# Kernel optimization log

Hardware: AMD Instinct MI355X
Metric: run time of the kernel (lower is better)

## Reference

```python
import jax, jax.numpy as jnp
import numpy as np
import math

B, S, D = 4, 2048, 1024

def setup_inputs() -> dict:
    key = jax.random.key(0)
    k1, k2, k3, k4 = jax.random.split(key, 4)
    scale = 1.0 / math.sqrt(D)
    return {
        "x": jax.random.normal(k1, (B, S, D), dtype=jnp.float32),
        "w_q": jax.random.normal(k2, (D, D), dtype=jnp.float32) * scale,
        "w_k": jax.random.normal(k3, (D, D), dtype=jnp.float32) * scale,
        "w_v": jax.random.normal(k4, (D, D), dtype=jnp.float32) * scale,
        "causal": 1,
    }

def reference(x, w_q, w_k, w_v, causal):
    # QKV projections: nn.Linear(dim, dim, bias=False) -> x @ W.T
    q = jnp.einsum('bsd,ed->bse', x, w_q)
    k = jnp.einsum('bsd,ed->bse', x, w_k)
    v = jnp.einsum('bsd,ed->bse', x, w_v)
    d_k = q.shape[-1]
    scores = jnp.einsum('bqd,bkd->bqk', q, k) / jnp.sqrt(jnp.asarray(d_k, q.dtype))
    if causal:
        seq_len = q.shape[-2]
        mask = jnp.triu(jnp.ones((seq_len, seq_len), dtype=bool), k=1)
        scores = jnp.where(mask, jnp.asarray(-jnp.inf, scores.dtype), scores)
    weights = jax.nn.softmax(scores, axis=-1)
    return jnp.einsum('bqk,bkd->bqd', weights, v)
```

## Files before the change

kernel.cpp:

```cpp
#include <hip/hip_runtime.h>
#include <stdint.h>

typedef unsigned short u16;
typedef __attribute__((ext_vector_type(8))) __bf16 bf16x8;
typedef __attribute__((ext_vector_type(4))) float f32x4;

__device__ __forceinline__ u16 f2bf(float f) {
  unsigned u = __float_as_uint(f);
  u += 0x7FFF + ((u >> 16) & 1);
  return (u16)(u >> 16);
}

__device__ __forceinline__ float bf2f(u16 h) {
  return __uint_as_float(((unsigned)h) << 16);
}

__device__ __forceinline__ void llds16(const u16* g, u16* l) {
  __builtin_amdgcn_global_load_lds(
      (const __attribute__((address_space(1))) void*)g,
      (__attribute__((address_space(3))) void*)l, 16, 0, 0);
}

__global__ __launch_bounds__(256) void cast_all(
    const float* __restrict__ x, const float* __restrict__ wq,
    const float* __restrict__ wk, const float* __restrict__ wv,
    u16* __restrict__ xb, u16* __restrict__ wb, float* __restrict__ lsum) {
  int i = blockIdx.x * 256 + threadIdx.x;
  if (i < 8192) lsum[i] = 0.f;
  const float* src; u16* dst; int off;
  if (i < 2097152)      { src = x;  dst = xb;            off = i; }
  else if (i < 2359296) { src = wq; dst = wb;            off = i - 2097152; }
  else if (i < 2621440) { src = wk; dst = wb + 1048576;  off = i - 2359296; }
  else                  { src = wv; dst = wb + 2097152;  off = i - 2621440; }
  float4 f = ((const float4*)src)[off];
  ushort4 o;
  o.x = f2bf(f.x); o.y = f2bf(f.y); o.z = f2bf(f.z); o.w = f2bf(f.w);
  ((ushort4*)dst)[off] = o;
}

template<int MODE>
__global__ __launch_bounds__(256) void gemm_nt(
    const u16* __restrict__ A, long long sA, int lda,
    const u16* __restrict__ B, long long sB, int ldb,
    void* __restrict__ Cp, long long sC, int ldc,
    int K, u16* __restrict__ vt, float scale,
    float* __restrict__ lsum, const int* __restrict__ causalp) {
  const int t = threadIdx.x;
  const int causal = (MODE == 0) ? 1 : causalp[0];

  int rt = blockIdx.x, ct = blockIdx.y, zb = blockIdx.z;
  if (MODE == 1) {
    const int xcd = blockIdx.x & 7;
    const int chunk = ((blockIdx.x >> 3) + 8 * blockIdx.z) & 31;
    if (chunk < 17) {
      int i2 = xcd * 17 + chunk, c = 0;
      while (i2 >= 16 - c) { i2 -= 16 - c; ++c; }
      ct = c; rt = c + i2;
    } else {
      if (causal) return;
      int i2 = xcd * 15 + (chunk - 17), r = 0;
      while (i2 >= r + 1) { i2 -= r + 1; ++r; }
      rt = i2; ct = r + 1;
    }
  }
  if (MODE == 2) {
    const int s = ((blockIdx.x & 7) << 6) + (blockIdx.x >> 3);
    zb = s >> 7;
    ct = (s & 127) >> 4;
    const int m = s & 15;
    rt = (s & 32) ? m : 15 - m;
  }

  const int rowbase = rt * 128;
  const int colbase = ct * 128;
  const u16* Ab = A + (long long)zb * sA;
  const u16* Bb = B + (long long)zb * sB;

  int Keff = K;
  if (MODE == 2 && causal) Keff = min(K, rowbase + 128);

  __shared__ u16 As[8192];
  __shared__ u16 Bs[8192];

  const int lane = t & 63;
  const int wv = t >> 6;
  const int wr = wv >> 1;
  const int wc = wv & 1;
  const int quad = lane >> 4;
  const int lr = lane & 15;

  f32x4 acc[4][4];
  const f32x4 zero = {0.f, 0.f, 0.f, 0.f};
#pragma unroll
  for (int i = 0; i < 4; ++i)
#pragma unroll
    for (int j = 0; j < 4; ++j) acc[i][j] = zero;

  {
    const int csw = (t & 7) ^ ((t >> 3) & 7);
    const u16* ga = Ab + (long long)(rowbase + (t >> 3)) * lda + csw * 8;
    const u16* gb = Bb + (long long)(colbase + (t >> 3)) * ldb + csw * 8;
    const long long ra = 32LL * lda, rb = 32LL * ldb;
    u16* la = As + t * 8;
    u16* lb = Bs + t * 8;

    const int m7 = lr & 7;
    const int a_base = (wr * 64 + lr) * 64 + ((quad ^ m7) * 8);
    const int b_base = (wc * 64 + lr) * 64 + ((quad ^ m7) * 8);

    for (int k0 = 0; k0 < Keff; k0 += 64) {
      __syncthreads();
#pragma unroll
      for (int i = 0; i < 4; ++i) {
        llds16(ga + k0 + i * ra, la + i * 2048);
        llds16(gb + k0 + i * rb, lb + i * 2048);
      }
      __syncthreads();
#pragma unroll
      for (int ks = 0; ks < 2; ++ks) {
        const int ko = ks ? 32 : 0;
        bf16x8 af[4], bfv[4];
#pragma unroll
        for (int tm = 0; tm < 4; ++tm)
          af[tm] = *(const bf16x8*)(As + ((a_base + tm * 1024) ^ ko));
#pragma unroll
        for (int tn = 0; tn < 4; ++tn)
          bfv[tn] = *(const bf16x8*)(Bs + ((b_base + tn * 1024) ^ ko));
#pragma unroll
        for (int tm = 0; tm < 4; ++tm)
#pragma unroll
          for (int tn = 0; tn < 4; ++tn)
            acc[tm][tn] = __builtin_amdgcn_mfma_f32_16x16x32_bf16(
                af[tm], bfv[tn], acc[tm][tn], 0, 0, 0);
      }
    }
  }

  if (MODE == 0 && colbase >= 2048) {
#pragma unroll
    for (int tm = 0; tm < 4; ++tm) {
      int s0 = rowbase + wr * 64 + tm * 16 + quad * 4;
      int b = s0 >> 11;
      int sl = s0 & 2047;
#pragma unroll
      for (int tn = 0; tn < 4; ++tn) {
        int e = colbase - 2048 + wc * 64 + tn * 16 + lr;
        ushort4 o;
        o.x = f2bf(acc[tm][tn][0]);
        o.y = f2bf(acc[tm][tn][1]);
        o.z = f2bf(acc[tm][tn][2]);
        o.w = f2bf(acc[tm][tn][3]);
        *(ushort4*)(vt + ((long long)(b * 1024 + e)) * 2048 + sl) = o;
      }
    }
    return;
  }

#pragma unroll
  for (int tm = 0; tm < 4; ++tm) {
#pragma unroll
    for (int r = 0; r < 4; ++r) {
      const int grow = rowbase + wr * 64 + tm * 16 + quad * 4 + r;
      float li, rsum = 0.f;
      if (MODE == 2) li = __builtin_amdgcn_rcpf(lsum[zb * 2048 + grow]);
#pragma unroll
      for (int tn = 0; tn < 4; ++tn) {
        const int gcol = colbase + wc * 64 + tn * 16 + lr;
        float val = acc[tm][tn][r];
        if (MODE == 0) {
          ((u16*)Cp)[(long long)grow * ldc + gcol] = f2bf(val);
        } else if (MODE == 1) {
          u16* C = (u16*)Cp + (long long)zb * sC;
          float ex = (causal && gcol > grow) ? 0.f : __expf(val * scale);
          C[(long long)grow * ldc + gcol] = f2bf(ex);
          rsum += ex;
        } else {
          float* C = (float*)Cp + (long long)zb * sC;
          C[(long long)grow * ldc + gcol] = val * li;
        }
      }
      if (MODE == 1) {
#pragma unroll
        for (int o = 8; o > 0; o >>= 1) rsum += __shfl_xor(rsum, o, 64);
        if (lr == 0)
          atomicAdd(&lsum[zb * 2048 + grow], rsum);
      }
    }
  }
}

extern "C" void kernel_launch(void* const* d_in, const int* in_sizes, int n_in,
                              void* d_out, int out_size, void* d_ws, size_t ws_size,
                              hipStream_t stream) {
  const float* x  = (const float*)d_in[0];
  const float* wq = (const float*)d_in[1];
  const float* wk = (const float*)d_in[2];
  const float* wv = (const float*)d_in[3];
  const int* causal = (const int*)d_in[4];
  float* out = (float*)d_out;

  char* ws = (char*)d_ws;
  u16* xb = (u16*)(ws);
  u16* wb = (u16*)(ws + 16777216);
  u16* qk = (u16*)(ws + 23068672);
  u16* vt = (u16*)(ws + 56623104);
  u16* sb = (u16*)(ws + 73400320);
  float* lsum = (float*)(ws + 106954752);

  cast_all<<<11264, 256, 0, stream>>>(x, wq, wk, wv, xb, wb, lsum);

  gemm_nt<0><<<dim3(64, 24, 1), 256, 0, stream>>>(
      xb, 0, 1024, wb, 0, 1024, qk, 0, 2048, 1024, vt, 1.0f, nullptr, causal);

  gemm_nt<1><<<dim3(256, 1, 4), 256, 0, stream>>>(
      qk, 2048LL * 2048, 2048, qk + 1024, 2048LL * 2048, 2048,
      sb, 2048LL * 2048, 2048, 1024, nullptr, 0.03125f, lsum, causal);

  gemm_nt<2><<<dim3(512, 1, 1), 256, 0, stream>>>(
      sb, 2048LL * 2048, 2048, vt, 1024LL * 2048, 2048,
      out, 2048LL * 1024, 1024, 2048, nullptr, 1.0f, lsum, causal);
}
```

Measured before the change: 223.2 us.

## Use atomic work-queue persistent blocks for causal score GEMM

Result: slower. 234.3 us (+5.0%).

```diff
diff --git a/kernel.cpp b/kernel.cpp
--- a/kernel.cpp
+++ b/kernel.cpp
@@ -24,9 +24,11 @@
 __global__ __launch_bounds__(256) void cast_all(
     const float* __restrict__ x, const float* __restrict__ wq,
     const float* __restrict__ wk, const float* __restrict__ wv,
-    u16* __restrict__ xb, u16* __restrict__ wb, float* __restrict__ lsum) {
+    u16* __restrict__ xb, u16* __restrict__ wb, float* __restrict__ lsum,
+    int* __restrict__ cnt) {
   int i = blockIdx.x * 256 + threadIdx.x;
   if (i < 8192) lsum[i] = 0.f;
+  if (i == 0) cnt[0] = 0;
   const float* src; u16* dst; int off;
   if (i < 2097152)      { src = x;  dst = xb;            off = i; }
   else if (i < 2359296) { src = wq; dst = wb;            off = i - 2097152; }
@@ -39,37 +41,13 @@
 }
 
 template<int MODE>
-__global__ __launch_bounds__(256) void gemm_nt(
+__device__ __forceinline__ void gemm_core(
+    int rt, int ct, int zb, int causal, u16* As, u16* Bs,
     const u16* __restrict__ A, long long sA, int lda,
     const u16* __restrict__ B, long long sB, int ldb,
     void* __restrict__ Cp, long long sC, int ldc,
-    int K, u16* __restrict__ vt, float scale,
-    float* __restrict__ lsum, const int* __restrict__ causalp) {
+    int K, u16* __restrict__ vt, float scale, float* __restrict__ lsum) {
   const int t = threadIdx.x;
-  const int causal = (MODE == 0) ? 1 : causalp[0];
-
-  int rt = blockIdx.x, ct = blockIdx.y, zb = blockIdx.z;
-  if (MODE == 1) {
-    const int xcd = blockIdx.x & 7;
-    const int chunk = ((blockIdx.x >> 3) + 8 * blockIdx.z) & 31;
-    if (chunk < 17) {
-      int i2 = xcd * 17 + chunk, c = 0;
-      while (i2 >= 16 - c) { i2 -= 16 - c; ++c; }
-      ct = c; rt = c + i2;
-    } else {
-      if (causal) return;
-      int i2 = xcd * 15 + (chunk - 17), r = 0;
-      while (i2 >= r + 1) { i2 -= r + 1; ++r; }
-      rt = i2; ct = r + 1;
-    }
-  }
-  if (MODE == 2) {
-    const int s = ((blockIdx.x & 7) << 6) + (blockIdx.x >> 3);
-    zb = s >> 7;
-    ct = (s & 127) >> 4;
-    const int m = s & 15;
-    rt = (s & 32) ? m : 15 - m;
-  }
 
   const int rowbase = rt * 128;
   const int colbase = ct * 128;
@@ -78,9 +56,6 @@
 
   int Keff = K;
   if (MODE == 2 && causal) Keff = min(K, rowbase + 128);
-
-  __shared__ u16 As[8192];
-  __shared__ u16 Bs[8192];
 
   const int lane = t & 63;
   const int wv = t >> 6;
@@ -189,6 +164,64 @@
   }
 }
 
+__global__ __launch_bounds__(256) void gemm_qkv(
+    const u16* __restrict__ xb, const u16* __restrict__ wb,
+    u16* __restrict__ qk, u16* __restrict__ vt) {
+  __shared__ u16 As[8192];
+  __shared__ u16 Bs[8192];
+  gemm_core<0>(blockIdx.x, blockIdx.y, 0, 1, As, Bs,
+               xb, 0, 1024, wb, 0, 1024, qk, 0, 2048, 1024, vt, 1.0f, nullptr);
+}
+
+__global__ __launch_bounds__(256) void gemm_sc(
+    const u16* __restrict__ qk, u16* __restrict__ sb,
+    float* __restrict__ lsum, const int* __restrict__ causalp,
+    int* __restrict__ cnt) {
+  __shared__ u16 As[8192];
+  __shared__ u16 Bs[8192];
+  __shared__ int jsh;
+  const int causal = causalp[0];
+  const int njobs = causal ? 544 : 1024;
+  for (;;) {
+    if (threadIdx.x == 0) jsh = atomicAdd(cnt, 1);
+    __syncthreads();
+    const int j = jsh;
+    if (j >= njobs) return;
+    int zb, rt, ct;
+    if (causal) {
+      zb = j / 136;
+      int i2 = j - zb * 136, r = 0;
+      while (i2 >= r + 1) { i2 -= r + 1; ++r; }
+      rt = r; ct = i2;
+    } else {
+      zb = j >> 8;
+      const int rem = j & 255;
+      rt = rem >> 4; ct = rem & 15;
+    }
+    gemm_core<1>(rt, ct, zb, causal, As, Bs,
+                 qk, 2048LL * 2048, 2048, qk + 1024, 2048LL * 2048, 2048,
+                 sb, 2048LL * 2048, 2048, 1024, nullptr, 0.03125f, lsum);
+    __syncthreads();
+  }
+}
+
+__global__ __launch_bounds__(256) void gemm_pv(
+    const u16* __restrict__ sb, const u16* __restrict__ vtb,
+    float* __restrict__ out, float* __restrict__ lsum,
+    const int* __restrict__ causalp) {
+  __shared__ u16 As[8192];
+  __shared__ u16 Bs[8192];
+  const int causal = causalp[0];
+  const int s = ((blockIdx.x & 7) << 6) + (blockIdx.x >> 3);
+  const int zb = s >> 7;
+  const int ct = (s & 127) >> 4;
+  const int m = s & 15;
+  const int rt = (s & 32) ? m : 15 - m;
+  gemm_core<2>(rt, ct, zb, causal, As, Bs,
+               sb, 2048LL * 2048, 2048, vtb, 1024LL * 2048, 2048,
+               out, 2048LL * 1024, 1024, 2048, nullptr, 1.0f, lsum);
+}
+
 extern "C" void kernel_launch(void* const* d_in, const int* in_sizes, int n_in,
                               void* d_out, int out_size, void* d_ws, size_t ws_size,
                               hipStream_t stream) {
@@ -206,17 +239,13 @@
   u16* vt = (u16*)(ws + 56623104);
   u16* sb = (u16*)(ws + 73400320);
   float* lsum = (float*)(ws + 106954752);
-
-  cast_all<<<11264, 256, 0, stream>>>(x, wq, wk, wv, xb, wb, lsum);
-
-  gemm_nt<0><<<dim3(64, 24, 1), 256, 0, stream>>>(
-      xb, 0, 1024, wb, 0, 1024, qk, 0, 2048, 1024, vt, 1.0f, nullptr, causal);
-
-  gemm_nt<1><<<dim3(256, 1, 4), 256, 0, stream>>>(
-      qk, 2048LL * 2048, 2048, qk + 1024, 2048LL * 2048, 2048,
-      sb, 2048LL * 2048, 2048, 1024, nullptr, 0.03125f, lsum, causal);
-
-  gemm_nt<2><<<dim3(512, 1, 1), 256, 0, stream>>>(
-      sb, 2048LL * 2048, 2048, vt, 1024LL * 2048, 2048,
-      out, 2048LL * 1024, 1024, 2048, nullptr, 1.0f, lsum, causal);
-}
+  int* cnt = (int*)out;
+
+  cast_all<<<11264, 256, 0, stream>>>(x, wq, wk, wv, xb, wb, lsum, cnt);
+
+  gemm_qkv<<<dim3(64, 24, 1), 256, 0, stream>>>(xb, wb, qk, vt);
+
+  gemm_sc<<<dim3(512, 1, 1), 256, 0, stream>>>(qk, sb, lsum, causal, cnt);
+
+  gemm_pv<<<dim3(512, 1, 1), 256, 0, stream>>>(sb, vt, out, lsum, causal);
+}
```
